# Kernel tuning notes

Hardware: AMD Instinct MI355X
Metric: run time of the kernel (lower is better)

## Reference

```python
import jax, jax.numpy as jnp
import numpy as np

B, S, HID = 1, 2048, 4096
NH, NKV, HD = 32, 8, 128
N_REP = NH // NKV
SCALING = HD ** -0.5
NEG_INF = jnp.float32(-jnp.inf)


def rotate_half(x):
    x1, x2 = jnp.split(x, 2, axis=-1)
    return jnp.concatenate((-x2, x1), axis=-1)


def setup_inputs() -> dict:
    key = jax.random.key(0)
    ks = jax.random.split(key, 8)
    hidden_states = jax.random.normal(ks[0], (B, S, HID), dtype=jnp.float32)
    # RoPE tables (uniform stand-ins; real cos/sin come from rotary embedding)
    pos = jnp.arange(S, dtype=jnp.float32)[:, None]
    inv_freq = 1.0 / (10000.0 ** (jnp.arange(0, HD, 2, dtype=jnp.float32) / HD))
    ang = pos * inv_freq[None, :]              # [S, HD/2]
    emb = jnp.concatenate([ang, ang], axis=-1)  # [S, HD]
    cos = jnp.cos(emb)[None].repeat(B, axis=0)  # [B, S, HD]
    sin = jnp.sin(emb)[None].repeat(B, axis=0)
    # HF-style additive causal mask: 0 on/below diagonal, -inf above
    tril = jnp.tril(jnp.ones((S, S), dtype=bool))
    attention_mask = jnp.where(tril, 0.0, NEG_INF).astype(jnp.float32)[None, None]  # [B,1,S,S]
    scale = 0.02
    q_w = jax.random.normal(ks[1], (HID, HID), dtype=jnp.float32) * scale
    k_w = jax.random.normal(ks[2], (NKV * HD, HID), dtype=jnp.float32) * scale
    v_w = jax.random.normal(ks[3], (NKV * HD, HID), dtype=jnp.float32) * scale
    o_w = jax.random.normal(ks[4], (HID, HID), dtype=jnp.float32) * scale
    return {"hidden_states": hidden_states, "cos": cos, "sin": sin,
            "attention_mask": attention_mask, "q_w": q_w, "k_w": k_w,
            "v_w": v_w, "o_w": o_w}


def reference(hidden_states, cos, sin, attention_mask, q_w, k_w, v_w, o_w):
    b, s, _ = hidden_states.shape
    # projections -> [B, H, S, D]
    q = (hidden_states @ q_w.T).reshape(b, s, NH, HD).transpose(0, 2, 1, 3)
    k = (hidden_states @ k_w.T).reshape(b, s, NKV, HD).transpose(0, 2, 1, 3)
    v = (hidden_states @ v_w.T).reshape(b, s, NKV, HD).transpose(0, 2, 1, 3)
    # RoPE (unsqueeze_dim=1)
    cos_u = cos[:, None, :, :]
    sin_u = sin[:, None, :, :]
    q = q * cos_u + rotate_half(q) * sin_u
    k = k * cos_u + rotate_half(k) * sin_u
    # repeat_kv (interleave each kv head n_rep times)
    k = jnp.repeat(k, N_REP, axis=1)
    v = jnp.repeat(v, N_REP, axis=1)
    attn = jnp.einsum("bhqd,bhkd->bhqk", q, k)
    # gen_mask: 0 -> 1, -inf -> 0 (passthrough otherwise)
    m = attention_mask
    mask01 = jnp.where(m == 0, 1.0, jnp.where(jnp.isneginf(m), 0.0, m))
    attn = attn * mask01
    causal = m[:, :, :, : k.shape[-2]]
    attn = (attn + causal) * SCALING
    probs = jax.nn.softmax(attn.astype(jnp.float32), axis=-1).astype(q.dtype)
    # dropout p=attention_dropout=0.0 in eval -> identity
    ctx = jnp.einsum("bhqk,bhkd->bhqd", probs, v)  # [B,H,S,D]
    out = ctx.transpose(0, 2, 1, 3).reshape(b, s, -1) @ o_w.T
    return out
```

## Files before the change

kernel.cpp:

```cpp
#include <hip/hip_runtime.h>


typedef __attribute__((ext_vector_type(8))) short bf16x8;
typedef __attribute__((ext_vector_type(4))) float f32x4;
typedef __attribute__((ext_vector_type(4))) unsigned short u16x4;

#define S_LEN 2048
#define HID 4096
#define NH 32
#define NKV 8
#define HD 128
#define KVDIM 1024
#define SCALING 0.08838834764831845f

__device__ inline unsigned short f2bf(float f) {
  unsigned u = __builtin_bit_cast(unsigned, f);
  u = (u + 0x7FFFu + ((u >> 16) & 1u)) >> 16;
  return (unsigned short)u;
}
__device__ inline unsigned short f2bf_fast(float f) {
  unsigned u = __builtin_bit_cast(unsigned, f);
  return (unsigned short)((u + 0x8000u) >> 16);
}
__device__ inline float bf2f(unsigned short h) {
  unsigned u = ((unsigned)h) << 16;
  return __builtin_bit_cast(float, u);
}

__device__ inline void gload_lds16(const unsigned short* g, unsigned short* l) {
  __builtin_amdgcn_global_load_lds(
      (const __attribute__((address_space(1))) void*)g,
      (__attribute__((address_space(3))) void*)l, 16, 0, 0);
}

#define SZ_HS (8388608u)
#define SZ_QW (16777216u)
#define SZ_KW (4194304u)
#define B0 SZ_HS
#define B1 (B0 + SZ_QW)
#define B2 (B1 + SZ_KW)
#define B3 (B2 + SZ_KW)
#define B4 (B3 + SZ_QW)

__global__ void cvt_all(const float* __restrict__ s0,
                        const float* __restrict__ s1,
                        const float* __restrict__ s2,
                        const float* __restrict__ s3,
                        const float* __restrict__ s4,
                        unsigned short* __restrict__ dst) {
  size_t i = ((size_t)blockIdx.x * blockDim.x + threadIdx.x) * 4;
  const float* src;
  size_t off;
  if (i < B0)      { src = s0; off = i; }
  else if (i < B1) { src = s1; off = i - B0; }
  else if (i < B2) { src = s2; off = i - B1; }
  else if (i < B3) { src = s3; off = i - B2; }
  else             { src = s4; off = i - B3; }
  f32x4 v = *(const f32x4*)(src + off);
  u16x4 o;
#pragma unroll
  for (int r = 0; r < 4; ++r) o[r] = f2bf(v[r]);
  *(u16x4*)(dst + i) = o;
}

__global__ __launch_bounds__(256, 3) void gemm_qkv(
    const unsigned short* __restrict__ A, const unsigned short* __restrict__ Bq_,
    const unsigned short* __restrict__ Bk_, const unsigned short* __restrict__ Bv_,
    const float* __restrict__ cosb, const float* __restrict__ sinb,
    unsigned short* __restrict__ Cq, unsigned short* __restrict__ Ck,
    unsigned short* __restrict__ Cvt) {
  __shared__ unsigned short As[2][128 * 32];
  __shared__ unsigned short Bs[2][128 * 32];
  const int K = HID;
  const int tid = threadIdx.x;
  const int lane = tid & 63;
  const int wave = tid >> 6;
  const int orig = blockIdx.y * gridDim.x + blockIdx.x;
  const int xcd = orig & 7, seq = orig >> 3;
  const int xt = xcd * ((int)gridDim.x >> 3) + (seq >> 4);
  const int yt = seq & 15;
  const int m0 = yt * 128;
  const int wr = wave >> 1, wc = wave & 1;
  const int lrow = lane & 15, lg = lane >> 4;

  const unsigned short* Bsel;
  if (xt < 32)      Bsel = Bq_ + (size_t)(xt * 128) * K;
  else if (xt < 40) Bsel = Bk_ + (size_t)((xt - 32) * 128) * K;
  else              Bsel = Bv_ + (size_t)((xt - 40) * 128) * K;

  const f32x4 zero = {0.f, 0.f, 0.f, 0.f};
  f32x4 acc[4][4];
#pragma unroll
  for (int i = 0; i < 4; ++i)
#pragma unroll
    for (int j = 0; j < 4; ++j) acc[i][j] = zero;

  const int r0s = tid >> 2, c0s = (tid & 3) * 8;
  const int r1s = (tid + 256) >> 2, c1s = ((tid + 256) & 3) * 8;
  const unsigned short* Ag0 = A + (size_t)(m0 + r0s) * K + c0s;
  const unsigned short* Ag1 = A + (size_t)(m0 + r1s) * K + c1s;
  const unsigned short* Bg0 = Bsel + (size_t)r0s * K + c0s;
  const unsigned short* Bg1 = Bsel + (size_t)r1s * K + c1s;
  unsigned short* Al0[2] = {&As[0][tid * 8], &As[1][tid * 8]};
  unsigned short* Al1[2] = {&As[0][(tid + 256) * 8], &As[1][(tid + 256) * 8]};
  unsigned short* Bl0[2] = {&Bs[0][tid * 8], &Bs[1][tid * 8]};
  unsigned short* Bl1[2] = {&Bs[0][(tid + 256) * 8], &Bs[1][(tid + 256) * 8]};

#define QKV_STAGE(buf, koff)                                                  \
  {                                                                           \
    gload_lds16(Ag0 + (koff), Al0[buf]);                                      \
    gload_lds16(Ag1 + (koff), Al1[buf]);                                      \
    gload_lds16(Bg0 + (koff), Bl0[buf]);                                      \
    gload_lds16(Bg1 + (koff), Bl1[buf]);                                      \
  }

  int colb[4];
#pragma unroll
  for (int j = 0; j < 4; ++j)
    colb[j] = wc * 32 + (j & 1) * 16 + (j >> 1) * 64;

  QKV_STAGE(0, 0);
  __syncthreads();
  int cur = 0;
  const int NT = K >> 5;
  for (int kt = 0; kt < NT; ++kt) {
    if (kt + 1 < NT) QKV_STAGE(cur ^ 1, (kt + 1) * 32);
    bf16x8 af[4], bq[4];
#pragma unroll
    for (int i = 0; i < 4; ++i)
      af[i] = *(const bf16x8*)(&As[cur][(wr * 64 + i * 16 + lrow) * 32 + lg * 8]);
#pragma unroll
    for (int j = 0; j < 4; ++j)
      bq[j] = *(const bf16x8*)(&Bs[cur][(colb[j] + lrow) * 32 + lg * 8]);
#pragma unroll
    for (int i = 0; i < 4; ++i)
#pragma unroll
      for (int j = 0; j < 4; ++j)
        acc[i][j] = __builtin_amdgcn_mfma_f32_16x16x32_bf16(af[i], bq[j],
                                                            acc[i][j], 0, 0, 0);
    __syncthreads();
    cur ^= 1;
  }
#undef QKV_STAGE

  if (xt < 40) {
    unsigned short* C = (xt < 32) ? Cq : Ck;
    const int ldc = (xt < 32) ? HID : KVDIM;
    const int n0 = (xt < 32) ? xt * 128 : (xt - 32) * 128;
#pragma unroll
    for (int i = 0; i < 4; ++i) {
#pragma unroll
      for (int jp = 0; jp < 2; ++jp) {
        const int d64 = wc * 32 + jp * 16 + lrow;
#pragma unroll
        for (int r = 0; r < 4; ++r) {
          const int s = m0 + wr * 64 + i * 16 + lg * 4 + r;
          const float cv = cosb[(size_t)s * 128 + d64];
          const float sv = sinb[(size_t)s * 128 + d64];
          const float lo = acc[i][jp][r], hi = acc[i][jp + 2][r];
          C[(size_t)s * ldc + n0 + d64]      = f2bf(lo * cv - hi * sv);
          C[(size_t)s * ldc + n0 + d64 + 64] = f2bf(hi * cv + lo * sv);
        }
      }
    }
  } else {
    const int n0 = (xt - 40) * 128;
#pragma unroll
    for (int i = 0; i < 4; ++i)
#pragma unroll
      for (int j = 0; j < 4; ++j) {
        const int mm = m0 + wr * 64 + i * 16 + lg * 4;
        const int nn = n0 + colb[j] + lrow;
        u16x4 pk;
#pragma unroll
        for (int r = 0; r < 4; ++r) pk[r] = f2bf(acc[i][j][r]);
        *(u16x4*)(Cvt + (size_t)nn * S_LEN + mm) = pk;
      }
  }
}

__global__ __launch_bounds__(256, 3) void gemm_o(
    const unsigned short* __restrict__ A, const unsigned short* __restrict__ B,
    float* __restrict__ C) {
  __shared__ unsigned short As[2][128 * 32];
  __shared__ unsigned short Bs[2][128 * 32];
  const int K = HID;
  const int tid = threadIdx.x;
  const int lane = tid & 63;
  const int wave = tid >> 6;
  const int orig = blockIdx.y * gridDim.x + blockIdx.x;
  const int xcd = orig & 7, seq = orig >> 3;
  const int xt = xcd * ((int)gridDim.x >> 3) + (seq >> 4);
  const int yt = seq & 15;
  const int m0 = yt * 128;
  const int n0 = xt * 128;
  const int wr = wave >> 1, wc = wave & 1;
  const int lrow = lane & 15, lg = lane >> 4;

  const f32x4 zero = {0.f, 0.f, 0.f, 0.f};
  f32x4 acc[4][4];
#pragma unroll
  for (int i = 0; i < 4; ++i)
#pragma unroll
    for (int j = 0; j < 4; ++j) acc[i][j] = zero;

  const int r0s = tid >> 2, c0s = (tid & 3) * 8;
  const int r1s = (tid + 256) >> 2, c1s = ((tid + 256) & 3) * 8;
  const unsigned short* Ag0 = A + (size_t)(m0 + r0s) * K + c0s;
  const unsigned short* Ag1 = A + (size_t)(m0 + r1s) * K + c1s;
  const unsigned short* Bg0 = B + (size_t)(n0 + r0s) * K + c0s;
  const unsigned short* Bg1 = B + (size_t)(n0 + r1s) * K + c1s;
  unsigned short* Al0[2] = {&As[0][tid * 8], &As[1][tid * 8]};
  unsigned short* Al1[2] = {&As[0][(tid + 256) * 8], &As[1][(tid + 256) * 8]};
  unsigned short* Bl0[2] = {&Bs[0][tid * 8], &Bs[1][tid * 8]};
  unsigned short* Bl1[2] = {&Bs[0][(tid + 256) * 8], &Bs[1][(tid + 256) * 8]};

#define O_STAGE(buf, koff)                                                    \
  {                                                                           \
    gload_lds16(Ag0 + (koff), Al0[buf]);                                      \
    gload_lds16(Ag1 + (koff), Al1[buf]);                                      \
    gload_lds16(Bg0 + (koff), Bl0[buf]);                                      \
    gload_lds16(Bg1 + (koff), Bl1[buf]);                                      \
  }

  O_STAGE(0, 0);
  __syncthreads();
  int cur = 0;
  const int NT = K >> 5;
  for (int kt = 0; kt < NT; ++kt) {
    if (kt + 1 < NT) O_STAGE(cur ^ 1, (kt + 1) * 32);
    bf16x8 af[4], bq[4];
#pragma unroll
    for (int i = 0; i < 4; ++i) {
      af[i] = *(const bf16x8*)(&As[cur][(wr * 64 + i * 16 + lrow) * 32 + lg * 8]);
      bq[i] = *(const bf16x8*)(&Bs[cur][(wc * 64 + i * 16 + lrow) * 32 + lg * 8]);
    }
#pragma unroll
    for (int i = 0; i < 4; ++i)
#pragma unroll
      for (int j = 0; j < 4; ++j)
        acc[i][j] = __builtin_amdgcn_mfma_f32_16x16x32_bf16(af[i], bq[j],
                                                            acc[i][j], 0, 0, 0);
    __syncthreads();
    cur ^= 1;
  }
#undef O_STAGE

#pragma unroll
  for (int i = 0; i < 4; ++i)
#pragma unroll
    for (int j = 0; j < 4; ++j) {
      const int mm = m0 + wr * 64 + i * 16 + lg * 4;
      const int nn = n0 + wc * 64 + j * 16 + lrow;
#pragma unroll
      for (int r = 0; r < 4; ++r)
        C[(size_t)(mm + r) * HID + nn] = acc[i][j][r];
    }
}

__global__ __launch_bounds__(256, 2) void attn_kernel(
    const unsigned short* __restrict__ Q, const unsigned short* __restrict__ Kc,
    const unsigned short* __restrict__ Vt, unsigned short* __restrict__ ctx) {
  __shared__ unsigned short Ks[2][64 * 128];
  __shared__ unsigned short Vs[2][128 * 64];
  __shared__ unsigned short Ps[4][16 * 72];
  const int tid = threadIdx.x;
  const int lane = tid & 63;
  const int wave = tid >> 6;
  const int h = blockIdx.x;
  const int hk = h >> 2;
  const int yl = (int)gridDim.y - 1 - blockIdx.y;
  const int r0 = yl * 128 + wave * 32;
  const int lrow = lane & 15, lg = lane >> 4;

  bf16x8 aq[2][4];
#pragma unroll
  for (int i = 0; i < 2; ++i) {
    const unsigned short* qb =
        Q + (size_t)(r0 + i * 16 + lrow) * HID + h * HD + lg * 8;
#pragma unroll
    for (int kk = 0; kk < 4; ++kk) aq[i][kk] = *(const bf16x8*)(qb + kk * 32);
  }

  const f32x4 zero = {0.f, 0.f, 0.f, 0.f};
  f32x4 o[2][8];
#pragma unroll
  for (int i = 0; i < 2; ++i)
#pragma unroll
    for (int t = 0; t < 8; ++t) o[i][t] = zero;
  f32x4 l_acc[2] = {zero, zero};
  float m_i[2][4];
#pragma unroll
  for (int i = 0; i < 2; ++i)
#pragma unroll
    for (int r = 0; r < 4; ++r) m_i[i][r] = -1e30f;

  const short onebf = (short)0x3F80;
  const bf16x8 onesf = {onebf, onebf, onebf, onebf, onebf, onebf, onebf, onebf};

  const unsigned short* Kg[4];
  const unsigned short* Vg[4];
  int Koff[4], Voff[4];
#pragma unroll
  for (int qq = 0; qq < 4; ++qq) {
    const int slot = tid + 256 * qq;
    {
      const int row = slot >> 4, ch = slot & 15;
      Kg[qq] = Kc + (size_t)row * KVDIM + hk * HD + ((ch ^ (row & 7)) * 8);
      Koff[qq] = slot * 8;
    }
    {
      const int row = slot >> 3, ch = slot & 7;
      Vg[qq] = Vt + ((size_t)hk * HD + row) * S_LEN + ((ch ^ (row & 7)) * 8);
      Voff[qq] = slot * 8;
    }
  }
  unsigned short* pw = &Ps[wave][0];

#pragma unroll
  for (int qq = 0; qq < 4; ++qq) gload_lds16(Kg[qq], &Ks[0][Koff[qq]]);
#pragma unroll
  for (int qq = 0; qq < 4; ++qq) gload_lds16(Vg[qq], &Vs[0][Voff[qq]]);
  __syncthreads();

  const int NTk = (yl * 128 + 128) >> 6;
  for (int t = 0; t < NTk; ++t) {
    const int k0 = t << 6;
    const int cur = t & 1;
    if (t + 1 < NTk) {
#pragma unroll
      for (int qq = 0; qq < 4; ++qq)
        gload_lds16(Kg[qq] + (size_t)(k0 + 64) * KVDIM, &Ks[cur ^ 1][Koff[qq]]);
#pragma unroll
      for (int qq = 0; qq < 4; ++qq)
        gload_lds16(Vg[qq] + (k0 + 64), &Vs[cur ^ 1][Voff[qq]]);
    }

    if (k0 <= r0 + 31) {
      f32x4 sacc[2][4];
#pragma unroll
      for (int i = 0; i < 2; ++i)
#pragma unroll
        for (int c = 0; c < 4; ++c) sacc[i][c] = zero;
#pragma unroll
      for (int c = 0; c < 4; ++c) {
        const int krow = c * 16 + lrow;
        bf16x8 bk[4];
#pragma unroll
        for (int kk = 0; kk < 4; ++kk)
          bk[kk] = *(const bf16x8*)(&Ks[cur][krow * 128 +
                                            (((kk * 4 + lg) ^ (krow & 7)) * 8)]);
#pragma unroll
        for (int i = 0; i < 2; ++i)
#pragma unroll
          for (int kk = 0; kk < 4; ++kk)
            sacc[i][c] = __builtin_amdgcn_mfma_f32_16x16x32_bf16(
                aq[i][kk], bk[kk], sacc[i][c], 0, 0, 0);
      }
      const bool full = (k0 + 63 <= r0);
#pragma unroll
      for (int i = 0; i < 2; ++i)
#pragma unroll
        for (int c = 0; c < 4; ++c)
#pragma unroll
          for (int r = 0; r < 4; ++r) {
            float v = sacc[i][c][r] * SCALING;
            if (!full) {
              const int row = r0 + i * 16 + lg * 4 + r;
              const int col = k0 + c * 16 + lrow;
              v = (col <= row) ? v : -1e30f;
            }
            sacc[i][c][r] = v;
          }
      float tm[2][4];
#pragma unroll
      for (int i = 0; i < 2; ++i)
#pragma unroll
        for (int r = 0; r < 4; ++r)
          tm[i][r] = fmaxf(fmaxf(sacc[i][0][r], sacc[i][1][r]),
                           fmaxf(sacc[i][2][r], sacc[i][3][r]));
#pragma unroll
      for (int mm = 1; mm < 16; mm <<= 1)
#pragma unroll
        for (int i = 0; i < 2; ++i)
#pragma unroll
          for (int r = 0; r < 4; ++r)
            tm[i][r] = fmaxf(tm[i][r], __shfl_xor(tm[i][r], mm, 64));
      bool grow = false;
#pragma unroll
      for (int i = 0; i < 2; ++i)
#pragma unroll
        for (int r = 0; r < 4; ++r) grow |= (tm[i][r] > m_i[i][r] + 8.0f);
      if (__any(grow)) {
        float sc[2][4];
#pragma unroll
        for (int i = 0; i < 2; ++i)
#pragma unroll
          for (int r = 0; r < 4; ++r) {
            const float mn = fmaxf(m_i[i][r], tm[i][r]);
            sc[i][r] = __expf(m_i[i][r] - mn);
            m_i[i][r] = mn;
          }
#pragma unroll
        for (int i = 0; i < 2; ++i) {
#pragma unroll
          for (int t2 = 0; t2 < 8; ++t2)
#pragma unroll
            for (int r = 0; r < 4; ++r) o[i][t2][r] *= sc[i][r];
#pragma unroll
          for (int r = 0; r < 4; ++r) l_acc[i][r] *= sc[i][r];
        }
      }
      bf16x8 pa[2][2];
#pragma unroll
      for (int i = 0; i < 2; ++i) {
#pragma unroll
        for (int c = 0; c < 4; ++c)
#pragma unroll
          for (int r = 0; r < 4; ++r)
            pw[(lg * 4 + r) * 72 + c * 16 + lrow] =
                f2bf_fast(__expf(sacc[i][c][r] - m_i[i][r]));
#pragma unroll
        for (int ks = 0; ks < 2; ++ks)
          pa[i][ks] = *(const bf16x8*)(pw + lrow * 72 + ks * 32 + lg * 8);
      }
#pragma unroll
      for (int i = 0; i < 2; ++i)
#pragma unroll
        for (int ks = 0; ks < 2; ++ks)
          l_acc[i] = __builtin_amdgcn_mfma_f32_16x16x32_bf16(pa[i][ks], onesf,
                                                             l_acc[i], 0, 0, 0);
#pragma unroll
      for (int t2 = 0; t2 < 8; ++t2) {
        const int vrow = t2 * 16 + lrow;
#pragma unroll
        for (int ks = 0; ks < 2; ++ks) {
          bf16x8 bv = *(const bf16x8*)(&Vs[cur][vrow * 64 +
                                               (((ks * 4 + lg) ^ (vrow & 7)) * 8)]);
#pragma unroll
          for (int i = 0; i < 2; ++i)
            o[i][t2] = __builtin_amdgcn_mfma_f32_16x16x32_bf16(pa[i][ks], bv,
                                                               o[i][t2], 0, 0, 0);
        }
      }
    }
    __syncthreads();
  }
  float inv[2][4];
#pragma unroll
  for (int i = 0; i < 2; ++i)
#pragma unroll
    for (int r = 0; r < 4; ++r) inv[i][r] = 1.f / l_acc[i][r];
#pragma unroll
  for (int i = 0; i < 2; ++i)
#pragma unroll
    for (int t = 0; t < 8; ++t)
#pragma unroll
      for (int r = 0; r < 4; ++r)
        ctx[(size_t)(r0 + i * 16 + lg * 4 + r) * HID + h * HD + t * 16 + lrow] =
            f2bf(o[i][t][r] * inv[i][r]);
}

extern "C" void kernel_launch(void* const* d_in, const int* in_sizes, int n_in,
                              void* d_out, int out_size, void* d_ws,
                              size_t ws_size, hipStream_t stream) {
  (void)in_sizes; (void)n_in; (void)out_size; (void)ws_size;
  const float* hs   = (const float*)d_in[0];
  const float* cosb = (const float*)d_in[1];
  const float* sinb = (const float*)d_in[2];
  const float* qw = (const float*)d_in[4];
  const float* kw = (const float*)d_in[5];
  const float* vw = (const float*)d_in[6];
  const float* ow = (const float*)d_in[7];
  float* out = (float*)d_out;

  unsigned short* ws = (unsigned short*)d_ws;
  unsigned short* hs_b = ws;
  unsigned short* qw_b = hs_b + SZ_HS;
  unsigned short* kw_b = qw_b + SZ_QW;
  unsigned short* vw_b = kw_b + SZ_KW;
  unsigned short* ow_b = vw_b + SZ_KW;
  unsigned short* q_b  = ow_b + SZ_QW;
  unsigned short* k_b  = q_b + SZ_HS;
  unsigned short* vt_b = k_b + (size_t)S_LEN * KVDIM;
  unsigned short* ctx_b = vt_b + (size_t)KVDIM * S_LEN;

  cvt_all<<<B4 / 1024, 256, 0, stream>>>(hs, qw, kw, vw, ow, hs_b);

  gemm_qkv<<<dim3(48, 16), 256, 0, stream>>>(hs_b, qw_b, kw_b, vw_b,
                                             cosb, sinb, q_b, k_b, vt_b);

  attn_kernel<<<dim3(NH, S_LEN / 128), 256, 0, stream>>>(q_b, k_b, vt_b, ctx_b);

  gemm_o<<<dim3(32, 16), 256, 0, stream>>>(ctx_b, ow_b, out);
}
```

Before: 352.0 us.

## Transpose QK^T MFMA so softmax row stats reduce in-lane with exp2

Swaps the MFMA operand order so each lane holds one query row's scores, which turns the row max into an in-lane reduction plus two cross-group shuffles instead of four-step butterfly shuffles over eight values. Scores are pre-scaled by scaling*log2(e) so the exponentials use exp2 directly. The row sum is accumulated in registers rather than through an extra ones-vector MFMA. The P tile is written to LDS as packed 4-wide vectors. In exchange, the rescale and final normalization need per-row shuffles to redistribute the factors to the output layout.

```diff
diff --git a/kernel.cpp b/kernel.cpp
--- a/kernel.cpp
+++ b/kernel.cpp
@@ -12,6 +12,8 @@
 #define HD 128
 #define KVDIM 1024
 #define SCALING 0.08838834764831845f
+#define ASC 0.12751744f
+#define THR2 11.5415603f
 
 __device__ inline unsigned short f2bf(float f) {
   unsigned u = __builtin_bit_cast(unsigned, f);
@@ -288,15 +290,8 @@
   for (int i = 0; i < 2; ++i)
 #pragma unroll
     for (int t = 0; t < 8; ++t) o[i][t] = zero;
-  f32x4 l_acc[2] = {zero, zero};
-  float m_i[2][4];
-#pragma unroll
-  for (int i = 0; i < 2; ++i)
-#pragma unroll
-    for (int r = 0; r < 4; ++r) m_i[i][r] = -1e30f;
-
-  const short onebf = (short)0x3F80;
-  const bf16x8 onesf = {onebf, onebf, onebf, onebf, onebf, onebf, onebf, onebf};
+  float l_i[2] = {0.f, 0.f};
+  float m_i[2] = {-1e30f, -1e30f};
 
   const unsigned short* Kg[4];
   const unsigned short* Vg[4];
@@ -355,81 +350,78 @@
 #pragma unroll
           for (int kk = 0; kk < 4; ++kk)
             sacc[i][c] = __builtin_amdgcn_mfma_f32_16x16x32_bf16(
-                aq[i][kk], bk[kk], sacc[i][c], 0, 0, 0);
+                bk[kk], aq[i][kk], sacc[i][c], 0, 0, 0);
       }
       const bool full = (k0 + 63 <= r0);
-#pragma unroll
-      for (int i = 0; i < 2; ++i)
+      float tm[2];
+#pragma unroll
+      for (int i = 0; i < 2; ++i) {
+        const int q = r0 + i * 16 + lrow;
 #pragma unroll
         for (int c = 0; c < 4; ++c)
 #pragma unroll
           for (int r = 0; r < 4; ++r) {
-            float v = sacc[i][c][r] * SCALING;
+            float v = sacc[i][c][r] * ASC;
             if (!full) {
-              const int row = r0 + i * 16 + lg * 4 + r;
-              const int col = k0 + c * 16 + lrow;
-              v = (col <= row) ? v : -1e30f;
+              const int k = k0 + c * 16 + lg * 4 + r;
+              v = (k <= q) ? v : -1e30f;
             }
             sacc[i][c][r] = v;
           }
-      float tm[2][4];
-#pragma unroll
-      for (int i = 0; i < 2; ++i)
-#pragma unroll
-        for (int r = 0; r < 4; ++r)
-          tm[i][r] = fmaxf(fmaxf(sacc[i][0][r], sacc[i][1][r]),
-                           fmaxf(sacc[i][2][r], sacc[i][3][r]));
-#pragma unroll
-      for (int mm = 1; mm < 16; mm <<= 1)
+        float m0v = fmaxf(fmaxf(sacc[i][0][0], sacc[i][0][1]),
+                          fmaxf(sacc[i][0][2], sacc[i][0][3]));
+        float m1v = fmaxf(fmaxf(sacc[i][1][0], sacc[i][1][1]),
+                          fmaxf(sacc[i][1][2], sacc[i][1][3]));
+        float m2v = fmaxf(fmaxf(sacc[i][2][0], sacc[i][2][1]),
+                          fmaxf(sacc[i][2][2], sacc[i][2][3]));
+        float m3v = fmaxf(fmaxf(sacc[i][3][0], sacc[i][3][1]),
+                          fmaxf(sacc[i][3][2], sacc[i][3][3]));
+        float tv = fmaxf(fmaxf(m0v, m1v), fmaxf(m2v, m3v));
+        tv = fmaxf(tv, __shfl_xor(tv, 16, 64));
+        tv = fmaxf(tv, __shfl_xor(tv, 32, 64));
+        tm[i] = tv;
+      }
+      const bool grow = (tm[0] > m_i[0] + THR2) || (tm[1] > m_i[1] + THR2);
+      if (__any(grow)) {
+        float scq[2];
+#pragma unroll
+        for (int i = 0; i < 2; ++i) {
+          const float mn = fmaxf(m_i[i], tm[i]);
+          scq[i] = __builtin_amdgcn_exp2f(m_i[i] - mn);
+          m_i[i] = mn;
+          l_i[i] *= scq[i];
+        }
 #pragma unroll
         for (int i = 0; i < 2; ++i)
 #pragma unroll
-          for (int r = 0; r < 4; ++r)
-            tm[i][r] = fmaxf(tm[i][r], __shfl_xor(tm[i][r], mm, 64));
-      bool grow = false;
-#pragma unroll
-      for (int i = 0; i < 2; ++i)
-#pragma unroll
-        for (int r = 0; r < 4; ++r) grow |= (tm[i][r] > m_i[i][r] + 8.0f);
-      if (__any(grow)) {
-        float sc[2][4];
-#pragma unroll
-        for (int i = 0; i < 2; ++i)
-#pragma unroll
           for (int r = 0; r < 4; ++r) {
-            const float mn = fmaxf(m_i[i][r], tm[i][r]);
-            sc[i][r] = __expf(m_i[i][r] - mn);
-            m_i[i][r] = mn;
+            const float scD = __shfl(scq[i], lg * 4 + r, 64);
+#pragma unroll
+            for (int t2 = 0; t2 < 8; ++t2) o[i][t2][r] *= scD;
           }
-#pragma unroll
-        for (int i = 0; i < 2; ++i) {
-#pragma unroll
-          for (int t2 = 0; t2 < 8; ++t2)
-#pragma unroll
-            for (int r = 0; r < 4; ++r) o[i][t2][r] *= sc[i][r];
-#pragma unroll
-          for (int r = 0; r < 4; ++r) l_acc[i][r] *= sc[i][r];
+      }
+      bf16x8 pa[2][2];
+#pragma unroll
+      for (int i = 0; i < 2; ++i) {
+        float rs = 0.f;
+#pragma unroll
+        for (int c = 0; c < 4; ++c) {
+          u16x4 pk;
+#pragma unroll
+          for (int r = 0; r < 4; ++r) {
+            const float p = __builtin_amdgcn_exp2f(sacc[i][c][r] - m_i[i]);
+            rs += p;
+            pk[r] = f2bf_fast(p);
+          }
+          *(u16x4*)(pw + lrow * 72 + c * 16 + lg * 4) = pk;
         }
-      }
-      bf16x8 pa[2][2];
-#pragma unroll
-      for (int i = 0; i < 2; ++i) {
-#pragma unroll
-        for (int c = 0; c < 4; ++c)
-#pragma unroll
-          for (int r = 0; r < 4; ++r)
-            pw[(lg * 4 + r) * 72 + c * 16 + lrow] =
-                f2bf_fast(__expf(sacc[i][c][r] - m_i[i][r]));
+        rs += __shfl_xor(rs, 16, 64);
+        rs += __shfl_xor(rs, 32, 64);
+        l_i[i] += rs;
 #pragma unroll
         for (int ks = 0; ks < 2; ++ks)
           pa[i][ks] = *(const bf16x8*)(pw + lrow * 72 + ks * 32 + lg * 8);
       }
-#pragma unroll
-      for (int i = 0; i < 2; ++i)
-#pragma unroll
-        for (int ks = 0; ks < 2; ++ks)
-          l_acc[i] = __builtin_amdgcn_mfma_f32_16x16x32_bf16(pa[i][ks], onesf,
-                                                             l_acc[i], 0, 0, 0);
 #pragma unroll
       for (int t2 = 0; t2 < 8; ++t2) {
         const int vrow = t2 * 16 + lrow;
@@ -446,19 +438,19 @@
     }
     __syncthreads();
   }
-  float inv[2][4];
+  float inv1[2];
+#pragma unroll
+  for (int i = 0; i < 2; ++i) inv1[i] = 1.f / l_i[i];
 #pragma unroll
   for (int i = 0; i < 2; ++i)
 #pragma unroll
-    for (int r = 0; r < 4; ++r) inv[i][r] = 1.f / l_acc[i][r];
-#pragma unroll
-  for (int i = 0; i < 2; ++i)
-#pragma unroll
-    for (int t = 0; t < 8; ++t)
-#pragma unroll
-      for (int r = 0; r < 4; ++r)
+    for (int r = 0; r < 4; ++r) {
+      const float invD = __shfl(inv1[i], lg * 4 + r, 64);
+#pragma unroll
+      for (int t = 0; t < 8; ++t)
         ctx[(size_t)(r0 + i * 16 + lg * 4 + r) * HID + h * HD + t * 16 + lrow] =
-            f2bf(o[i][t][r] * inv[i][r]);
+            f2bf(o[i][t][r] * invD);
+    }
 }
 
 extern "C" void kernel_launch(void* const* d_in, const int* in_sizes, int n_in,
```

New measurement: 334.5 us. -5.0%, faster.
